# Kernel tuning notes

Hardware: AMD Instinct MI355X
Metric: run time of the kernel (lower is better)

The kernel has to match this reference:

```python
import jax, jax.numpy as jnp
import numpy as np

V, E = 32000, 256
B, S = 8, 512
NA, NC, NS = 12, 24, 576  # N_AXIOMS, N_COMPOSITES, N_STATE
DECAY = 0.9
EPS = 1e-5


def _xavier(key, shape):
    fan_in, fan_out = shape[0], shape[1]
    lim = np.sqrt(6.0 / (fan_in + fan_out))
    return jax.random.uniform(key, shape, jnp.float32, -lim, lim)


def setup_inputs() -> dict:
    key = jax.random.key(0)
    ks = jax.random.split(key, 8)
    return {
        "input_ids": jax.random.randint(ks[0], (B, S), 0, V),
        "embed_table": 0.02 * jax.random.normal(ks[1], (V, E), jnp.float32),
        "ax_w": _xavier(ks[2], (E, NA)), "ax_b": jnp.zeros((NA,), jnp.float32),
        "ax_g": jnp.ones((NA,), jnp.float32), "ax_beta": jnp.zeros((NA,), jnp.float32),
        "comp_w": _xavier(ks[3], (NA, NC)), "comp_b": jnp.zeros((NC,), jnp.float32),
        "comp_g": jnp.ones((NC,), jnp.float32), "comp_beta": jnp.zeros((NC,), jnp.float32),
        "mix": jnp.asarray(0.1, jnp.float32),
        "out_w1": _xavier(ks[4], (NS, 512)), "out_b1": jnp.zeros((512,), jnp.float32),
        "out_w2": _xavier(ks[5], (512, V)), "out_b2": jnp.zeros((V,), jnp.float32),
    }


def _ln(x, g, b):
    m = jnp.mean(x, axis=-1, keepdims=True)
    v = jnp.var(x, axis=-1, keepdims=True)
    return (x - m) * jax.lax.rsqrt(v + EPS) * g + b


def reference(input_ids, embed_table, ax_w, ax_b, ax_g, ax_beta,
              comp_w, comp_b, comp_g, comp_beta, mix,
              out_w1, out_b1, out_w2, out_b2):
    # Embedding lookup (dropout is identity at eval)
    embeds = embed_table[input_ids]                              # [B,S,E]
    # The axiom/composite branches have no time dependence -> compute all steps at once
    axioms = jnp.tanh(_ln(embeds @ ax_w + ax_b, ax_g, ax_beta))  # [B,S,12]
    comps = jnp.tanh(_ln(axioms @ comp_w + comp_b, comp_g, comp_beta))  # [B,S,24]

    sig_mix = jax.nn.sigmoid(mix)
    state0 = jnp.zeros((input_ids.shape[0], NC, NC), jnp.float32)

    def step(state, c):  # c: [B,24]
        state = DECAY * state + sig_mix * (c[:, :, None] * c[:, None, :])
        h = jax.nn.gelu(state.reshape(state.shape[0], NS) @ out_w1 + out_b1,
                        approximate=False)
        logits = h @ out_w2 + out_b2                             # [B,V]
        return state, logits

    final_state, logits = jax.lax.scan(step, state0, jnp.swapaxes(comps, 0, 1))
    return jnp.swapaxes(logits, 0, 1), final_state               # [B,S,V], [B,24,24]
```

## Files before the change

### kernel.cpp

```cpp
#include <hip/hip_runtime.h>
#include <hip/hip_bf16.h>
#include <math.h>

#define BB 8
#define SS 512
#define VV 32000
#define EE 256
#define NAx 12
#define NCc 24
#define NSt 576
#define MM (BB*SS)

typedef __bf16 bf16x8 __attribute__((ext_vector_type(8)));
typedef float f32x4 __attribute__((ext_vector_type(4)));

#define MFMA16(a, b, c) __builtin_amdgcn_mfma_f32_16x16x32_bf16((a), (b), (c), 0, 0, 0)

__device__ __forceinline__ void gl2lds16(const void* g, void* l) {
  __builtin_amdgcn_global_load_lds(
      (const __attribute__((address_space(1))) void*)g,
      (__attribute__((address_space(3))) void*)l, 16, 0, 0);
}

#define FENCE() asm volatile("" ::: "memory")
#define BAR()   do { FENCE(); __builtin_amdgcn_s_barrier(); FENCE(); } while (0)

__global__ __launch_bounds__(256) void k_transpose_w2(
    const float* __restrict__ in, __hip_bfloat16* __restrict__ out)
{
  __shared__ __hip_bfloat16 tb[64][260];
  const int tid = threadIdx.x;
  const int c0 = blockIdx.x * 64;
  const int r0 = blockIdx.y * 256;
  const int rr = tid >> 4;
  const int cc = (tid & 15) * 4;
#pragma unroll
  for (int p = 0; p < 16; ++p) {
    const int r = p * 16 + rr;
    float4 v = *(const float4*)&in[(size_t)(r0 + r) * 32000 + c0 + cc];
    tb[cc + 0][r] = __float2bfloat16(v.x);
    tb[cc + 1][r] = __float2bfloat16(v.y);
    tb[cc + 2][r] = __float2bfloat16(v.z);
    tb[cc + 3][r] = __float2bfloat16(v.w);
  }
  __syncthreads();
  const int w = tid >> 6, lane = tid & 63;
#pragma unroll
  for (int q = 0; q < 16; ++q) {
    const int c = q * 4 + w;
    ushort4 u = *(const ushort4*)&tb[c][lane * 4];
    *(ushort4*)&out[(size_t)(c0 + c) * 512 + r0 + lane * 4] = u;
  }
}

__global__ __launch_bounds__(256) void k_transpose64(
    const float* __restrict__ in, __hip_bfloat16* __restrict__ out, int R, int C)
{
  __shared__ float t[64][65];
  const int tx = threadIdx.x, ty = threadIdx.y;
  const int c0 = blockIdx.x * 64, r0 = blockIdx.y * 64;
#pragma unroll
  for (int i = 0; i < 64; i += 4)
    t[ty + i][tx] = in[(size_t)(r0 + ty + i) * C + (c0 + tx)];
  __syncthreads();
#pragma unroll
  for (int i = 0; i < 64; i += 4)
    out[(size_t)(c0 + ty + i) * R + (r0 + tx)] = __float2bfloat16(t[tx][ty + i]);
}

__global__ __launch_bounds__(64) void k_embed_comps(
    const int* __restrict__ ids, const float* __restrict__ ET,
    const float* __restrict__ axw, const float* __restrict__ axb,
    const float* __restrict__ axg, const float* __restrict__ axbeta,
    const float* __restrict__ cw,  const float* __restrict__ cb,
    const float* __restrict__ cg,  const float* __restrict__ cbeta,
    float* __restrict__ comps)
{
  __shared__ float sw[EE * NAx];
  __shared__ float scw[NAx * NCc];
  const int tid = threadIdx.x;
  for (int i = tid; i < EE * NAx; i += 64) sw[i] = axw[i];
  for (int i = tid; i < NAx * NCc; i += 64) scw[i] = cw[i];
  __syncthreads();

  const int m = blockIdx.x * 64 + tid;
  const int id = ids[m];
  const float4* e4 = reinterpret_cast<const float4*>(ET + (size_t)id * EE);

  float a[NAx];
#pragma unroll
  for (int t = 0; t < NAx; ++t) a[t] = axb[t];

  for (int q = 0; q < EE / 4; ++q) {
    float4 v = e4[q];
#pragma unroll
    for (int c = 0; c < 4; ++c) {
      float x = (c == 0) ? v.x : (c == 1) ? v.y : (c == 2) ? v.z : v.w;
      const float* wrow = &sw[(q * 4 + c) * NAx];
#pragma unroll
      for (int t = 0; t < NAx; ++t) a[t] += x * wrow[t];
    }
  }
  {
    float mean = 0.f;
#pragma unroll
    for (int t = 0; t < NAx; ++t) mean += a[t];
    mean *= (1.0f / NAx);
    float var = 0.f;
#pragma unroll
    for (int t = 0; t < NAx; ++t) { float d = a[t] - mean; var += d * d; }
    var *= (1.0f / NAx);
    float rs = rsqrtf(var + 1e-5f);
#pragma unroll
    for (int t = 0; t < NAx; ++t)
      a[t] = tanhf((a[t] - mean) * rs * axg[t] + axbeta[t]);
  }
  float c24[NCc];
#pragma unroll
  for (int j = 0; j < NCc; ++j) c24[j] = cb[j];
#pragma unroll
  for (int t = 0; t < NAx; ++t) {
    float x = a[t];
    const float* wrow = &scw[t * NCc];
#pragma unroll
    for (int j = 0; j < NCc; ++j) c24[j] += x * wrow[j];
  }
  {
    float mean = 0.f;
#pragma unroll
    for (int j = 0; j < NCc; ++j) mean += c24[j];
    mean *= (1.0f / NCc);
    float var = 0.f;
#pragma unroll
    for (int j = 0; j < NCc; ++j) { float d = c24[j] - mean; var += d * d; }
    var *= (1.0f / NCc);
    float rs = rsqrtf(var + 1e-5f);
#pragma unroll
    for (int j = 0; j < NCc; ++j)
      c24[j] = tanhf((c24[j] - mean) * rs * cg[j] + cbeta[j]);
  }
#pragma unroll
  for (int j = 0; j < NCc; ++j) comps[(size_t)m * NCc + j] = c24[j];
}

__global__ __launch_bounds__(576) void k_recurrence(
    const float* __restrict__ comps, const float* __restrict__ mix,
    __hip_bfloat16* __restrict__ ST, float* __restrict__ fstate)
{
  __shared__ float sc[SS * NCc];
  const int b = blockIdx.x, tid = threadIdx.x;
  const float* src = comps + (size_t)b * SS * NCc;
  for (int i = tid; i < SS * NCc; i += 576) sc[i] = src[i];
  __syncthreads();

  const float sm = 1.0f / (1.0f + expf(-mix[0]));
  const int i = tid / NCc, j = tid - i * NCc;
  float st = 0.0f;
  __hip_bfloat16* stp = ST + (size_t)b * SS * NSt + tid;
  float ci = sc[i], cj = sc[j];
#pragma unroll 4
  for (int t = 0; t < SS; ++t) {
    const int tn = t + 1;
    float nci = (tn < SS) ? sc[tn * NCc + i] : 0.f;
    float ncj = (tn < SS) ? sc[tn * NCc + j] : 0.f;
    st = 0.9f * st + sm * ci * cj;
    stp[(size_t)t * NSt] = __float2bfloat16(st);
    ci = nci; cj = ncj;
  }
  fstate[b * NSt + tid] = st;
}

__global__ __launch_bounds__(256) void k_gemm_bt_gelu(
    const __hip_bfloat16* __restrict__ A,
    const __hip_bfloat16* __restrict__ Bt,
    const float* __restrict__ bias,
    __hip_bfloat16* __restrict__ Cb,
    int M, int N, int K)
{
  __shared__ __align__(16) __hip_bfloat16 As[128 * 32];
  __shared__ __align__(16) __hip_bfloat16 Bs[128 * 32];
  const int tid  = threadIdx.x;
  const int lane = tid & 63;
  const int w    = tid >> 6;
  const int wr   = w >> 1, wc = w & 1;
  const int m0 = blockIdx.y * 128;
  const int n0 = blockIdx.x * 128;
  const int lr = lane & 15;
  const int kb = lane >> 4;

  f32x4 acc[4][4];
#pragma unroll
  for (int i = 0; i < 4; ++i)
#pragma unroll
    for (int j = 0; j < 4; ++j) acc[i][j] = (f32x4){0.f, 0.f, 0.f, 0.f};

  for (int k0 = 0; k0 < K; k0 += 32) {
    __syncthreads();
#pragma unroll
    for (int p = 0; p < 2; ++p) {
      const int lbase = w * 2048 + p * 1024;
      const int o  = lbase + lane * 16;
      const int r  = o >> 6;
      const int sg = (o >> 4) & 3;
      gl2lds16(A  + (size_t)(m0 + r) * K + k0 + sg * 8, (char*)As + lbase);
      gl2lds16(Bt + (size_t)(n0 + r) * K + k0 + sg * 8, (char*)Bs + lbase);
    }
    asm volatile("s_waitcnt vmcnt(0)" ::: "memory");
    __syncthreads();

    bf16x8 af[4], bv[4];
#pragma unroll
    for (int mr = 0; mr < 4; ++mr)
      af[mr] = *reinterpret_cast<const bf16x8*>(&As[(wr * 64 + mr * 16 + lr) * 32 + kb * 8]);
#pragma unroll
    for (int nr = 0; nr < 4; ++nr)
      bv[nr] = *reinterpret_cast<const bf16x8*>(&Bs[(wc * 64 + nr * 16 + lr) * 32 + kb * 8]);
#pragma unroll
    for (int mr = 0; mr < 4; ++mr)
#pragma unroll
      for (int nr = 0; nr < 4; ++nr)
        acc[mr][nr] = MFMA16(af[mr], bv[nr], acc[mr][nr]);
  }

#pragma unroll
  for (int nr = 0; nr < 4; ++nr) {
    const int col = n0 + wc * 64 + nr * 16 + lr;
    const float bvs = bias[col];
#pragma unroll
    for (int mr = 0; mr < 4; ++mr) {
      const int rbase = m0 + wr * 64 + mr * 16 + kb * 4;
#pragma unroll
      for (int r = 0; r < 4; ++r) {
        float v = acc[mr][nr][r] + bvs;
        v = 0.5f * v * (1.0f + erff(v * 0.70710678118654752f));
        Cb[(size_t)(rbase + r) * N + col] = __float2bfloat16(v);
      }
    }
  }
}

__global__ __launch_bounds__(256, 2) void k_gemm2_128(
    const __hip_bfloat16* __restrict__ A,
    const __hip_bfloat16* __restrict__ Bt,
    const float* __restrict__ bias,
    float* __restrict__ C,
    int M, int N, int K, int tiles_m)
{
  __shared__ __align__(16) char smem[65536];

  const int NK  = K >> 6;
  const int tid = threadIdx.x;
  const int lane = tid & 63;
  const int w  = tid >> 6;
  const int wr = w >> 1;
  const int wc = w & 1;
  const int lr = lane & 15;
  const int kb = lane >> 4;

  const int nwg = gridDim.x;
  const int cpx = nwg >> 3;
  const int s   = ((int)blockIdx.x & 7) * cpx + ((int)blockIdx.x >> 3);
  const int nt  = s / tiles_m;
  const int mt  = s - nt * tiles_m;
  const int m0  = mt << 7;
  const int n0  = nt << 7;

  const int srow = tid >> 3;
  const int scol = ((tid & 7) ^ (srow & 7)) << 3;
  const int swz0 = (kb ^ (lr & 7)) << 4;
  const int swz1 = swz0 ^ 64;

#define STAGE_A(buf, R, tk0)                                              \
  gl2lds16(A + (size_t)(m0 + (R) + srow) * K + (tk0) + scol,              \
           smem + (buf)*16384 + (R)*128 + w*1024)
#define STAGE_B(buf, R, tk0)                                              \
  gl2lds16(Bt + (size_t)(n0 + (R) + srow) * K + (tk0) + scol,             \
           smem + 32768 + (buf)*16384 + (R)*128 + w*1024)

#define LDA(buf, mf, kh) \
  (*(const bf16x8*)(smem + (buf)*16384 + (wr*64 + (mf)*16 + lr)*128 + ((kh) ? swz1 : swz0)))
#define LDB(buf, nf, kh) \
  (*(const bf16x8*)(smem + 32768 + (buf)*16384 + (wc*64 + (nf)*16 + lr)*128 + ((kh) ? swz1 : swz0)))

  f32x4 acc[4][4];
#pragma unroll
  for (int i = 0; i < 4; ++i)
#pragma unroll
    for (int j = 0; j < 4; ++j) acc[i][j] = (f32x4){0.f, 0.f, 0.f, 0.f};

  float bvs[4];
#pragma unroll
  for (int nf = 0; nf < 4; ++nf) bvs[nf] = bias[n0 + wc * 64 + nf * 16 + lr];

  STAGE_A(0, 0, 0);  STAGE_A(0, 32, 0);  STAGE_A(0, 64, 0);  STAGE_A(0, 96, 0);
  STAGE_B(0, 0, 0);  STAGE_B(0, 32, 0);  STAGE_B(0, 64, 0);  STAGE_B(0, 96, 0);
  STAGE_B(1, 0, 64); STAGE_B(1, 32, 64); STAGE_B(1, 64, 64); STAGE_B(1, 96, 64);
  asm volatile("s_waitcnt vmcnt(4)" ::: "memory");
  BAR();

#pragma unroll 1
  for (int t = 0; t < NK; ++t) {
    const int c  = t & 1;
    const int k1 = (t + 1) << 6;
    const int k2 = (t + 2) << 6;
    bf16x8 a0[4], b0[4], a1[4], b1[4];

#pragma unroll
    for (int mf = 0; mf < 4; ++mf) a0[mf] = LDA(c, mf, 0);
#pragma unroll
    for (int nf = 0; nf < 4; ++nf) b0[nf] = LDB(c, nf, 0);
    if (t < NK - 1) { STAGE_A(c ^ 1, 0, k1); STAGE_A(c ^ 1, 32, k1); }
    BAR();
    asm volatile("s_waitcnt lgkmcnt(0)" ::: "memory");
    __builtin_amdgcn_sched_barrier(0);
    __builtin_amdgcn_s_setprio(1);
#pragma unroll
    for (int mf = 0; mf < 4; ++mf) {
      acc[mf][0] = MFMA16(a0[mf], b0[0], acc[mf][0]);
      acc[mf][1] = MFMA16(a0[mf], b0[1], acc[mf][1]);
    }
    __builtin_amdgcn_s_setprio(0);
    BAR();

#pragma unroll
    for (int mf = 0; mf < 4; ++mf) a1[mf] = LDA(c, mf, 1);
#pragma unroll
    for (int nf = 0; nf < 4; ++nf) b1[nf] = LDB(c, nf, 1);
    if (t < NK - 1) { STAGE_A(c ^ 1, 64, k1); STAGE_A(c ^ 1, 96, k1); }
    BAR();
    asm volatile("s_waitcnt lgkmcnt(0)" ::: "memory");
    __builtin_amdgcn_sched_barrier(0);
    __builtin_amdgcn_s_setprio(1);
#pragma unroll
    for (int mf = 0; mf < 4; ++mf) {
      acc[mf][2] = MFMA16(a0[mf], b0[2], acc[mf][2]);
      acc[mf][3] = MFMA16(a0[mf], b0[3], acc[mf][3]);
    }
    __builtin_amdgcn_s_setprio(0);
    BAR();

    if (t < NK - 2) { STAGE_B(c, 0, k2); STAGE_B(c, 32, k2); }
    BAR();
    __builtin_amdgcn_s_setprio(1);
#pragma unroll
    for (int mf = 0; mf < 4; ++mf) {
      acc[mf][0] = MFMA16(a1[mf], b1[0], acc[mf][0]);
      acc[mf][1] = MFMA16(a1[mf], b1[1], acc[mf][1]);
    }
    __builtin_amdgcn_s_setprio(0);
    BAR();

    if (t < NK - 2) { STAGE_B(c, 64, k2); STAGE_B(c, 96, k2); }
    BAR();
    __builtin_amdgcn_s_setprio(1);
#pragma unroll
    for (int mf = 0; mf < 4; ++mf) {
      acc[mf][2] = MFMA16(a1[mf], b1[2], acc[mf][2]);
      acc[mf][3] = MFMA16(a1[mf], b1[3], acc[mf][3]);
    }
    __builtin_amdgcn_s_setprio(0);
    if (t < NK - 2) {
      asm volatile("s_waitcnt vmcnt(4)" ::: "memory");
    } else if (t == NK - 2) {
      asm volatile("s_waitcnt vmcnt(0)" ::: "memory");
    }
    BAR();
  }

  float* ls = (float*)smem;
#pragma unroll
  for (int mf = 0; mf < 4; ++mf) {
#pragma unroll
    for (int nf = 0; nf < 4; ++nf) {
      const int col = wc * 64 + nf * 16 + lr;
#pragma unroll
      for (int r = 0; r < 4; ++r) {
        const int row = wr * 64 + mf * 16 + kb * 4 + r;
        const int seg = (col >> 2) ^ (row & 7);
        ls[row * 128 + seg * 4 + (col & 3)] = acc[mf][nf][r] + bvs[nf];
      }
    }
  }
  asm volatile("s_waitcnt lgkmcnt(0)" ::: "memory");
  BAR();
#pragma unroll
  for (int pass = 0; pass < 16; ++pass) {
    const int lrow = pass * 8 + w * 2 + (lane >> 5);
    const int seg  = (lane & 31) ^ (lrow & 7);
    f32x4 v = *(const f32x4*)&ls[lrow * 128 + seg * 4];
    __builtin_nontemporal_store(v,
        (f32x4*)&C[(size_t)(m0 + lrow) * N + n0 + (lane & 31) * 4]);
  }
#undef STAGE_A
#undef STAGE_B
#undef LDA
#undef LDB
}

extern "C" void kernel_launch(void* const* d_in, const int* in_sizes, int n_in,
                              void* d_out, int out_size, void* d_ws, size_t ws_size,
                              hipStream_t stream) {
  const int*   ids  = (const int*)  d_in[0];
  const float* ET   = (const float*)d_in[1];
  const float* axw  = (const float*)d_in[2];
  const float* axb  = (const float*)d_in[3];
  const float* axg  = (const float*)d_in[4];
  const float* axbt = (const float*)d_in[5];
  const float* cw   = (const float*)d_in[6];
  const float* cb   = (const float*)d_in[7];
  const float* cg   = (const float*)d_in[8];
  const float* cbt  = (const float*)d_in[9];
  const float* mix  = (const float*)d_in[10];
  const float* w1   = (const float*)d_in[11];
  const float* b1   = (const float*)d_in[12];
  const float* w2   = (const float*)d_in[13];
  const float* b2   = (const float*)d_in[14];

  float* out = (float*)d_out;

  char* ws = (char*)d_ws;
  size_t o = 0;
  __hip_bfloat16* W2T   = (__hip_bfloat16*)(ws + o); o += (size_t)VV * 512 * 2;
  __hip_bfloat16* W1T   = (__hip_bfloat16*)(ws + o); o += (size_t)512 * NSt * 2;
  float*          comps = (float*)(ws + o);          o += (size_t)MM * NCc * 4;
  __hip_bfloat16* STb   = (__hip_bfloat16*)(ws + o); o += (size_t)MM * NSt * 2;
  __hip_bfloat16* H     = (__hip_bfloat16*)(ws + o); o += (size_t)MM * 512 * 2;

  k_transpose_w2<<<dim3(VV / 64, 2), 256, 0, stream>>>(w2, W2T);
  k_transpose64<<<dim3(512 / 64, NSt / 64), dim3(64, 4), 0, stream>>>(w1, W1T, NSt, 512);

  k_embed_comps<<<MM / 64, 64, 0, stream>>>(ids, ET, axw, axb, axg, axbt,
                                            cw, cb, cg, cbt, comps);

  k_recurrence<<<BB, NSt, 0, stream>>>(comps, mix, STb, out + (size_t)MM * VV);

  k_gemm_bt_gelu<<<dim3(512 / 128, MM / 128), 256, 0, stream>>>(
      STb, W1T, b1, H, MM, 512, NSt);

  k_gemm2_128<<<(VV / 128) * (MM / 128), 256, 0, stream>>>(
      H, W2T, b2, out, MM, VV, 512, MM / 128);
}
```

Before: 276.8 us.

## Fuse prep kernels into one launch and chunk recurrence over time with warmup

Merges the two weight transposes and the embedding/composite computation into a single kernel dispatched by block index, removing launch gaps. Splits the sequential recurrence into four time chunks per batch, each recomputing the state over the prior 128 steps as warmup, raising parallelism from 8 to 32 blocks. The warmup truncates older history, relying on the 0.9 decay to make the omitted contribution negligible, and adds redundant recurrence work.

After: 263.8 us. -4.7%, faster.

```diff
diff --git a/kernel.cpp b/kernel.cpp
--- a/kernel.cpp
+++ b/kernel.cpp
@@ -25,50 +25,9 @@
 #define FENCE() asm volatile("" ::: "memory")
 #define BAR()   do { FENCE(); __builtin_amdgcn_s_barrier(); FENCE(); } while (0)
 
-__global__ __launch_bounds__(256) void k_transpose_w2(
-    const float* __restrict__ in, __hip_bfloat16* __restrict__ out)
-{
-  __shared__ __hip_bfloat16 tb[64][260];
-  const int tid = threadIdx.x;
-  const int c0 = blockIdx.x * 64;
-  const int r0 = blockIdx.y * 256;
-  const int rr = tid >> 4;
-  const int cc = (tid & 15) * 4;
-#pragma unroll
-  for (int p = 0; p < 16; ++p) {
-    const int r = p * 16 + rr;
-    float4 v = *(const float4*)&in[(size_t)(r0 + r) * 32000 + c0 + cc];
-    tb[cc + 0][r] = __float2bfloat16(v.x);
-    tb[cc + 1][r] = __float2bfloat16(v.y);
-    tb[cc + 2][r] = __float2bfloat16(v.z);
-    tb[cc + 3][r] = __float2bfloat16(v.w);
-  }
-  __syncthreads();
-  const int w = tid >> 6, lane = tid & 63;
-#pragma unroll
-  for (int q = 0; q < 16; ++q) {
-    const int c = q * 4 + w;
-    ushort4 u = *(const ushort4*)&tb[c][lane * 4];
-    *(ushort4*)&out[(size_t)(c0 + c) * 512 + r0 + lane * 4] = u;
-  }
-}
-
-__global__ __launch_bounds__(256) void k_transpose64(
-    const float* __restrict__ in, __hip_bfloat16* __restrict__ out, int R, int C)
-{
-  __shared__ float t[64][65];
-  const int tx = threadIdx.x, ty = threadIdx.y;
-  const int c0 = blockIdx.x * 64, r0 = blockIdx.y * 64;
-#pragma unroll
-  for (int i = 0; i < 64; i += 4)
-    t[ty + i][tx] = in[(size_t)(r0 + ty + i) * C + (c0 + tx)];
-  __syncthreads();
-#pragma unroll
-  for (int i = 0; i < 64; i += 4)
-    out[(size_t)(c0 + ty + i) * R + (r0 + tx)] = __float2bfloat16(t[tx][ty + i]);
-}
-
-__global__ __launch_bounds__(64) void k_embed_comps(
+__global__ __launch_bounds__(256) void k_prep(
+    const float* __restrict__ w2, __hip_bfloat16* __restrict__ W2T,
+    const float* __restrict__ w1, __hip_bfloat16* __restrict__ W1T,
     const int* __restrict__ ids, const float* __restrict__ ET,
     const float* __restrict__ axw, const float* __restrict__ axb,
     const float* __restrict__ axg, const float* __restrict__ axbeta,
@@ -76,98 +35,150 @@
     const float* __restrict__ cg,  const float* __restrict__ cbeta,
     float* __restrict__ comps)
 {
-  __shared__ float sw[EE * NAx];
-  __shared__ float scw[NAx * NCc];
-  const int tid = threadIdx.x;
-  for (int i = tid; i < EE * NAx; i += 64) sw[i] = axw[i];
-  for (int i = tid; i < NAx * NCc; i += 64) scw[i] = cw[i];
-  __syncthreads();
-
-  const int m = blockIdx.x * 64 + tid;
-  const int id = ids[m];
-  const float4* e4 = reinterpret_cast<const float4*>(ET + (size_t)id * EE);
-
-  float a[NAx];
-#pragma unroll
-  for (int t = 0; t < NAx; ++t) a[t] = axb[t];
-
-  for (int q = 0; q < EE / 4; ++q) {
-    float4 v = e4[q];
-#pragma unroll
-    for (int c = 0; c < 4; ++c) {
-      float x = (c == 0) ? v.x : (c == 1) ? v.y : (c == 2) ? v.z : v.w;
-      const float* wrow = &sw[(q * 4 + c) * NAx];
-#pragma unroll
-      for (int t = 0; t < NAx; ++t) a[t] += x * wrow[t];
-    }
-  }
-  {
-    float mean = 0.f;
-#pragma unroll
-    for (int t = 0; t < NAx; ++t) mean += a[t];
-    mean *= (1.0f / NAx);
-    float var = 0.f;
-#pragma unroll
-    for (int t = 0; t < NAx; ++t) { float d = a[t] - mean; var += d * d; }
-    var *= (1.0f / NAx);
-    float rs = rsqrtf(var + 1e-5f);
-#pragma unroll
-    for (int t = 0; t < NAx; ++t)
-      a[t] = tanhf((a[t] - mean) * rs * axg[t] + axbeta[t]);
-  }
-  float c24[NCc];
-#pragma unroll
-  for (int j = 0; j < NCc; ++j) c24[j] = cb[j];
-#pragma unroll
-  for (int t = 0; t < NAx; ++t) {
-    float x = a[t];
-    const float* wrow = &scw[t * NCc];
-#pragma unroll
-    for (int j = 0; j < NCc; ++j) c24[j] += x * wrow[j];
-  }
-  {
-    float mean = 0.f;
-#pragma unroll
-    for (int j = 0; j < NCc; ++j) mean += c24[j];
-    mean *= (1.0f / NCc);
-    float var = 0.f;
-#pragma unroll
-    for (int j = 0; j < NCc; ++j) { float d = c24[j] - mean; var += d * d; }
-    var *= (1.0f / NCc);
-    float rs = rsqrtf(var + 1e-5f);
-#pragma unroll
-    for (int j = 0; j < NCc; ++j)
-      c24[j] = tanhf((c24[j] - mean) * rs * cg[j] + cbeta[j]);
-  }
-#pragma unroll
-  for (int j = 0; j < NCc; ++j) comps[(size_t)m * NCc + j] = c24[j];
+  __shared__ __align__(16) char smu[33280];
+  const int bid = blockIdx.x, tid = threadIdx.x;
+
+  if (bid < 1000) {
+    __hip_bfloat16 (*tb)[260] = (__hip_bfloat16 (*)[260])smu;
+    const int c0 = (bid % 500) * 64;
+    const int r0 = (bid / 500) * 256;
+    const int rr = tid >> 4;
+    const int cc = (tid & 15) * 4;
+#pragma unroll
+    for (int p = 0; p < 16; ++p) {
+      const int r = p * 16 + rr;
+      float4 v = *(const float4*)&w2[(size_t)(r0 + r) * 32000 + c0 + cc];
+      tb[cc + 0][r] = __float2bfloat16(v.x);
+      tb[cc + 1][r] = __float2bfloat16(v.y);
+      tb[cc + 2][r] = __float2bfloat16(v.z);
+      tb[cc + 3][r] = __float2bfloat16(v.w);
+    }
+    __syncthreads();
+    const int w = tid >> 6, lane = tid & 63;
+#pragma unroll
+    for (int q = 0; q < 16; ++q) {
+      const int c = q * 4 + w;
+      ushort4 u = *(const ushort4*)&tb[c][lane * 4];
+      *(ushort4*)&W2T[(size_t)(c0 + c) * 512 + r0 + lane * 4] = u;
+    }
+  } else if (bid < 1072) {
+    float (*t)[65] = (float (*)[65])smu;
+    const int idx = bid - 1000;
+    const int bx = idx & 7;
+    const int by = idx >> 3;
+    const int tx = tid & 63, ty = tid >> 6;
+    const int c0 = bx * 64, r0 = by * 64;
+#pragma unroll
+    for (int i = 0; i < 64; i += 4)
+      t[ty + i][tx] = w1[(size_t)(r0 + ty + i) * 512 + c0 + tx];
+    __syncthreads();
+#pragma unroll
+    for (int i = 0; i < 64; i += 4)
+      W1T[(size_t)(c0 + ty + i) * 576 + r0 + tx] = __float2bfloat16(t[tx][ty + i]);
+  } else {
+    float* sw  = (float*)smu;
+    float* scw = sw + EE * NAx;
+    for (int i = tid; i < EE * NAx; i += 256) sw[i] = axw[i];
+    for (int i = tid; i < NAx * NCc; i += 256) scw[i] = cw[i];
+    __syncthreads();
+
+    const int m = (bid - 1072) * 256 + tid;
+    const int id = ids[m];
+    const float4* e4 = reinterpret_cast<const float4*>(ET + (size_t)id * EE);
+
+    float a[NAx];
+#pragma unroll
+    for (int t = 0; t < NAx; ++t) a[t] = axb[t];
+
+    for (int q = 0; q < EE / 4; ++q) {
+      float4 v = e4[q];
+#pragma unroll
+      for (int c = 0; c < 4; ++c) {
+        float x = (c == 0) ? v.x : (c == 1) ? v.y : (c == 2) ? v.z : v.w;
+        const float* wrow = &sw[(q * 4 + c) * NAx];
+#pragma unroll
+        for (int t = 0; t < NAx; ++t) a[t] += x * wrow[t];
+      }
+    }
+    {
+      float mean = 0.f;
+#pragma unroll
+      for (int t = 0; t < NAx; ++t) mean += a[t];
+      mean *= (1.0f / NAx);
+      float var = 0.f;
+#pragma unroll
+      for (int t = 0; t < NAx; ++t) { float d = a[t] - mean; var += d * d; }
+      var *= (1.0f / NAx);
+      float rs = rsqrtf(var + 1e-5f);
+#pragma unroll
+      for (int t = 0; t < NAx; ++t)
+        a[t] = tanhf((a[t] - mean) * rs * axg[t] + axbeta[t]);
+    }
+    float c24[NCc];
+#pragma unroll
+    for (int j = 0; j < NCc; ++j) c24[j] = cb[j];
+#pragma unroll
+    for (int t = 0; t < NAx; ++t) {
+      float x = a[t];
+      const float* wrow = &scw[t * NCc];
+#pragma unroll
+      for (int j = 0; j < NCc; ++j) c24[j] += x * wrow[j];
+    }
+    {
+      float mean = 0.f;
+#pragma unroll
+      for (int j = 0; j < NCc; ++j) mean += c24[j];
+      mean *= (1.0f / NCc);
+      float var = 0.f;
+#pragma unroll
+      for (int j = 0; j < NCc; ++j) { float d = c24[j] - mean; var += d * d; }
+      var *= (1.0f / NCc);
+      float rs = rsqrtf(var + 1e-5f);
+#pragma unroll
+      for (int j = 0; j < NCc; ++j)
+        c24[j] = tanhf((c24[j] - mean) * rs * cg[j] + cbeta[j]);
+    }
+#pragma unroll
+    for (int j = 0; j < NCc; ++j) comps[(size_t)m * NCc + j] = c24[j];
+  }
 }
 
 __global__ __launch_bounds__(576) void k_recurrence(
     const float* __restrict__ comps, const float* __restrict__ mix,
     __hip_bfloat16* __restrict__ ST, float* __restrict__ fstate)
 {
-  __shared__ float sc[SS * NCc];
-  const int b = blockIdx.x, tid = threadIdx.x;
-  const float* src = comps + (size_t)b * SS * NCc;
-  for (int i = tid; i < SS * NCc; i += 576) sc[i] = src[i];
+  __shared__ float sc[256 * NCc];
+  const int bid = blockIdx.x;
+  const int b = bid >> 2, c = bid & 3;
+  const int tid = threadIdx.x;
+  const int ts = c * 128;
+  const int t0 = (c == 0) ? 0 : ts - 128;
+  const int rows = ts + 128 - t0;
+
+  const float* src = comps + ((size_t)b * SS + t0) * NCc;
+  for (int i = tid; i < rows * NCc; i += 576) sc[i] = src[i];
   __syncthreads();
 
-  const float sm = 1.0f / (1.0f + expf(-mix[0]));
+  const float sm_ = 1.0f / (1.0f + expf(-mix[0]));
   const int i = tid / NCc, j = tid - i * NCc;
   float st = 0.0f;
-  __hip_bfloat16* stp = ST + (size_t)b * SS * NSt + tid;
-  float ci = sc[i], cj = sc[j];
+
+  const int warm = rows - 128;
+  for (int t = 0; t < warm; ++t)
+    st = 0.9f * st + sm_ * sc[t * NCc + i] * sc[t * NCc + j];
+
+  __hip_bfloat16* stp = ST + ((size_t)b * SS + ts) * NSt + tid;
+  float ci = sc[warm * NCc + i], cj = sc[warm * NCc + j];
 #pragma unroll 4
-  for (int t = 0; t < SS; ++t) {
-    const int tn = t + 1;
-    float nci = (tn < SS) ? sc[tn * NCc + i] : 0.f;
-    float ncj = (tn < SS) ? sc[tn * NCc + j] : 0.f;
-    st = 0.9f * st + sm * ci * cj;
+  for (int t = 0; t < 128; ++t) {
+    const int tn = warm + t + 1;
+    float nci = (t < 127) ? sc[tn * NCc + i] : 0.f;
+    float ncj = (t < 127) ? sc[tn * NCc + j] : 0.f;
+    st = 0.9f * st + sm_ * ci * cj;
     stp[(size_t)t * NSt] = __float2bfloat16(st);
     ci = nci; cj = ncj;
   }
-  fstate[b * NSt + tid] = st;
+  if (c == 3) fstate[b * NSt + tid] = st;
 }
 
 __global__ __launch_bounds__(256) void k_gemm_bt_gelu(
@@ -426,13 +437,11 @@
   __hip_bfloat16* STb   = (__hip_bfloat16*)(ws + o); o += (size_t)MM * NSt * 2;
   __hip_bfloat16* H     = (__hip_bfloat16*)(ws + o); o += (size_t)MM * 512 * 2;
 
-  k_transpose_w2<<<dim3(VV / 64, 2), 256, 0, stream>>>(w2, W2T);
-  k_transpose64<<<dim3(512 / 64, NSt / 64), dim3(64, 4), 0, stream>>>(w1, W1T, NSt, 512);
-
-  k_embed_comps<<<MM / 64, 64, 0, stream>>>(ids, ET, axw, axb, axg, axbt,
-                                            cw, cb, cg, cbt, comps);
-
-  k_recurrence<<<BB, NSt, 0, stream>>>(comps, mix, STb, out + (size_t)MM * VV);
+  k_prep<<<1088, 256, 0, stream>>>(w2, W2T, w1, W1T, ids, ET,
+                                   axw, axb, axg, axbt,
+                                   cw, cb, cg, cbt, comps);
+
+  k_recurrence<<<32, NSt, 0, stream>>>(comps, mix, STb, out + (size_t)MM * VV);
 
   k_gemm_bt_gelu<<<dim3(512 / 128, MM / 128), 256, 0, stream>>>(
       STb, W1T, b1, H, MM, 512, NSt);
```
